# Optimization experiments

Hardware: AMD Instinct MI355X
Metric: run time of the kernel (lower is better)

Reference implementation:

```python
import jax, jax.numpy as jnp
import numpy as np

SCENE_BOUND = 1.5
INV_SCALE = 1.0 / (2.0 * np.sqrt(2.0))  # (1/sqrt(2))^3 per 3D haar synthesis step


def idwt3_haar(approx, details):
    """One level of 3D inverse Haar DWT.

    approx:  (C, D, D, D)   'aaa' subband
    details: (7, C, D, D, D) subbands in ptwt key order
             ('aad','ada','add','daa','dad','dda','ddd')
    returns: (C, 2D, 2D, 2D)
    """
    C, D = approx.shape[0], approx.shape[1]
    # Stack 8 subbands; key order is lexicographic in (a=0, d=1) per axis,
    # so reshape to a (2,2,2) subband grid indexed (b_depth, b_height, b_width).
    coeffs = jnp.concatenate([approx[None], details], axis=0).reshape(2, 2, 2, C, D, D, D)
    # Haar synthesis signs: approx contributes +1 to both output phases,
    # detail contributes +1 to even phase, -1 to odd phase.
    S = jnp.array([[1.0, 1.0], [1.0, -1.0]], dtype=approx.dtype)
    out = jnp.einsum('uvwcijk,up,vq,wr->cipjqkr', coeffs, S, S, S) * jnp.asarray(INV_SCALE, approx.dtype)
    return out.reshape(C, 2 * D, 2 * D, 2 * D)


def trilinear_query(vol, xyz, bound):
    """torch grid_sample(mode='bilinear', padding='zeros', align_corners=True).

    vol: (C, R, R, R) with dims (D, H, W); xyz: (N, 3) world coords,
    columns (x, y, z) index (W, H, D) respectively.
    returns: (N, C)
    """
    C, R = vol.shape[0], vol.shape[1]
    g = xyz / bound                                # normalized to [-1, 1]
    pix = (g + 1.0) * 0.5 * (R - 1)                # align_corners=True mapping
    i0 = jnp.floor(pix).astype(jnp.int32)
    frac = pix - i0.astype(vol.dtype)
    x0, y0, z0 = i0[:, 0], i0[:, 1], i0[:, 2]
    fx, fy, fz = frac[:, 0], frac[:, 1], frac[:, 2]

    def gather(ix, iy, iz):
        valid = ((ix >= 0) & (ix < R) & (iy >= 0) & (iy < R) & (iz >= 0) & (iz < R))
        v = vol[:, jnp.clip(iz, 0, R - 1), jnp.clip(iy, 0, R - 1), jnp.clip(ix, 0, R - 1)]  # (C, N)
        return v * valid.astype(vol.dtype)

    out = jnp.zeros((C, xyz.shape[0]), dtype=vol.dtype)
    for dz in (0, 1):
        wz = fz if dz else 1.0 - fz
        for dy in (0, 1):
            wy = fy if dy else 1.0 - fy
            for dx in (0, 1):
                wx = fx if dx else 1.0 - fx
                out = out + gather(x0 + dx, y0 + dy, z0 + dz) * (wx * wy * wz)
    return out.T  # (N, C)


def setup_inputs() -> dict:
    key = jax.random.key(0)
    k0, k1, k2, k3, k4 = jax.random.split(key, 5)
    C = 28
    approx = jax.random.normal(k0, (C, 16, 16, 16), dtype=jnp.float32) * 0.01
    details_0 = jax.random.normal(k1, (7, C, 16, 16, 16), dtype=jnp.float32) * 0.001
    details_1 = jax.random.normal(k2, (7, C, 32, 32, 32), dtype=jnp.float32) * 0.001
    details_2 = jax.random.normal(k3, (7, C, 64, 64, 64), dtype=jnp.float32) * 0.001
    xyz = (jax.random.uniform(k4, (1_000_000, 3), dtype=jnp.float32) * 2.0 - 1.0) * SCENE_BOUND
    return {"approx": approx, "details_0": details_0, "details_1": details_1,
            "details_2": details_2, "xyz": xyz}


def reference(approx, details_0, details_1, details_2, xyz):
    # reconstruct(max_level=None): incremental multi-level IDWT synthesis
    vol = approx
    for d in (details_0, details_1, details_2):
        vol = idwt3_haar(vol, d)          # (C, 32^3) -> (C, 64^3) -> (C, 128^3)
    # query(): trilinear interpolation at world-space points
    return trilinear_query(vol, xyz, SCENE_BOUND)  # (N, C)
```

## Files before the change

kernel.cpp:

```cpp
#include <hip/hip_runtime.h>
#include <hip/hip_fp16.h>

#define INVS 0.35355339059327373f
#define CCH 28
#define QRS 127

__device__ __forceinline__ void haar8(const float c[8], float o[8]) {
    float t00p = c[0] + c[1], t00m = c[0] - c[1];
    float t01p = c[2] + c[3], t01m = c[2] - c[3];
    float t10p = c[4] + c[5], t10m = c[4] - c[5];
    float t11p = c[6] + c[7], t11m = c[6] - c[7];
    float u00p = t00p + t01p, u00m = t00m + t01m;
    float u01p = t00p - t01p, u01m = t00m - t01m;
    float u10p = t10p + t11p, u10m = t10m + t11m;
    float u11p = t10p - t11p, u11m = t10m - t11m;
    o[0] = (u00p + u10p) * INVS;  o[1] = (u00m + u10m) * INVS;
    o[2] = (u01p + u11p) * INVS;  o[3] = (u01m + u11m) * INVS;
    o[4] = (u00p - u10p) * INVS;  o[5] = (u00m - u10m) * INVS;
    o[6] = (u01p - u11p) * INVS;  o[7] = (u01m - u11m) * INVS;
}

__device__ __forceinline__ float3 pixcoord(float x, float y, float z) {
    const float R1 = 63.5f, IB = 1.0f / 1.5f;
    float3 p;
    p.x = __fmul_rn(__fadd_rn(__fmul_rn(x, IB), 1.0f), R1);
    p.y = __fmul_rn(__fadd_rn(__fmul_rn(y, IB), 1.0f), R1);
    p.z = __fmul_rn(__fadd_rn(__fmul_rn(z, IB), 1.0f), R1);
    return p;
}
__device__ __forceinline__ int cell_of(float3 p) {
    int cx = min(max((int)floorf(p.x), 0), 127) >> 3;
    int cy = min(max((int)floorf(p.y), 0), 127) >> 3;
    int cz = min(max((int)floorf(p.z), 0), 127) >> 2;
    return (cz * 16 + cy) * 16 + cx;
}

template <int LOGD, typename TA>
__global__ void idwt_cf_h(const TA* __restrict__ approx,
                          const float* __restrict__ details,
                          __half* __restrict__ out) {
    constexpr int D  = 1 << LOGD;
    constexpr int D3 = D * D * D;
    int t  = blockIdx.x * blockDim.x + threadIdx.x;
    int xc = t & (D - 1);
    int yc = (t >> LOGD) & (D - 1);
    int zc = (t >> (2 * LOGD)) & (D - 1);
    int c  = t >> (3 * LOGD);
    if (c >= CCH) return;
    int base = c * D3 + ((zc * D + yc) * D + xc);
    float cf[8];
    cf[0] = (float)approx[base];
#pragma unroll
    for (int j = 0; j < 7; ++j) cf[j + 1] = details[j * (CCH * D3) + base];
    float o[8];
    haar8(cf, o);
    constexpr int D2 = 2 * D;
    __half2* outv = (__half2*)out;
    int ob = (((c * D2 + 2 * zc) * D2 + 2 * yc) * D + xc);
    __half2 h01, h23, h45, h67;
    h01.x = __float2half(o[0]); h01.y = __float2half(o[1]);
    h23.x = __float2half(o[2]); h23.y = __float2half(o[3]);
    h45.x = __float2half(o[4]); h45.y = __float2half(o[5]);
    h67.x = __float2half(o[6]); h67.y = __float2half(o[7]);
    outv[ob]              = h01;
    outv[ob + D]          = h23;
    outv[ob + D2 * D]     = h45;
    outv[ob + D2 * D + D] = h67;
}

__global__ void __launch_bounds__(256) idwt_last(const __half* __restrict__ vol1,
                                                 const float* __restrict__ details,
                                                 __half* __restrict__ out) {
    constexpr int D3 = 64 * 64 * 64;
    __shared__ unsigned short lds[4 * CCH * 130];
    int zc = blockIdx.x >> 6, yc = blockIdx.x & 63;
    int rowc = (zc * 64 + yc) * 64;
#pragma unroll 1
    for (int it = 0; it < 7; ++it) {
        int item = it * 256 + threadIdx.x;
        int c = item >> 6, xc = item & 63;
        int base = c * D3 + rowc + xc;
        float cf[8];
        cf[0] = (float)vol1[base];
#pragma unroll
        for (int j = 0; j < 7; ++j) cf[j + 1] = details[j * (CCH * D3) + base];
        float o[8];
        haar8(cf, o);
#pragma unroll
        for (int k = 0; k < 8; ++k) {
            int p2q = k >> 1, r = k & 1;
            lds[(p2q * CCH + c) * 130 + 2 * xc + r] = __half_as_ushort(__float2half(o[k]));
        }
    }
    __syncthreads();
#pragma unroll 1
    for (int it = 0; it < 7; ++it) {
        int t2 = it * 256 + threadIdx.x;
        int plane = t2 / 448;
        int rem = t2 - plane * 448;
        int p = plane >> 1, q = plane & 1;
        unsigned int h[8];
#pragma unroll
        for (int j = 0; j < 8; ++j) {
            int f = rem * 8 + j;
            int vox = f / 28;
            int ch = f - 28 * vox;
            h[j] = lds[(plane * CCH + ch) * 130 + vox];
        }
        uint4 r4;
        r4.x = h[0] | (h[1] << 16);
        r4.y = h[2] | (h[3] << 16);
        r4.z = h[4] | (h[5] << 16);
        r4.w = h[6] | (h[7] << 16);
        long orow = ((long)(2 * zc + p) * 128 + (2 * yc + q)) * (128 * CCH);
        ((uint4*)(out + orow))[rem] = r4;
    }
}

__global__ void hist_k(const float* __restrict__ xyz, int* __restrict__ hist, int N) {
    int i = blockIdx.x * 256 + threadIdx.x;
    if (i >= N) return;
    float3 p = pixcoord(xyz[3 * i], xyz[3 * i + 1], xyz[3 * i + 2]);
    atomicAdd(&hist[cell_of(p)], 1);
}

__global__ void __launch_bounds__(256) scan_k(const int* __restrict__ hist,
                                              int* __restrict__ off,
                                              int* __restrict__ cursor) {
    __shared__ int part[256];
    int t = threadIdx.x;
    int loc[32], s = 0;
#pragma unroll
    for (int i = 0; i < 32; ++i) { loc[i] = s; s += hist[t * 32 + i]; }
    part[t] = s;
    __syncthreads();
    for (int d = 1; d < 256; d <<= 1) {
        int v = (t >= d) ? part[t - d] : 0;
        __syncthreads();
        part[t] += v;
        __syncthreads();
    }
    int excl = part[t] - s;
#pragma unroll
    for (int i = 0; i < 32; ++i) {
        int o = excl + loc[i];
        off[t * 32 + i] = o;
        cursor[t * 32 + i] = o;
    }
    if (t == 255) off[8192] = part[255];
}

__global__ void scatter_k(const float* __restrict__ xyz, int* __restrict__ cursor,
                          float4* __restrict__ recs, int N) {
    int i = blockIdx.x * 256 + threadIdx.x;
    if (i >= N) return;
    float3 p = pixcoord(xyz[3 * i], xyz[3 * i + 1], xyz[3 * i + 2]);
    int cell = cell_of(p);
    int pos = atomicAdd(&cursor[cell], 1);
    recs[pos] = make_float4(__int_as_float(i), p.x, p.y, p.z);
}

__global__ void __launch_bounds__(256, 7) query_cell(const float4* __restrict__ recs,
                                                     const int* __restrict__ off,
                                                     const __half* __restrict__ vol,
                                                     float* __restrict__ out) {
    __shared__ unsigned int lds[45 * QRS];
    int cell = blockIdx.x;
    int cx = cell & 15, cy = (cell >> 4) & 15, cz = cell >> 8;
    const unsigned int* vd = (const unsigned int*)vol;
    const long VOLDW = 128L * 128 * 128 * 14;
    for (int e = threadIdx.x; e < 45 * 63; e += 256) {
        int row = e / 63;
        int k2  = e - row * 63;
        int lz = row / 9, ly = row - 9 * lz;
        int gz = min(4 * cz + lz, 127), gy = min(8 * cy + ly, 127);
        long g = ((long)(gz * 128 + gy) * 128 + 8 * cx) * 14 + 2 * k2;
        g = min(g, VOLDW - 2);
        uint2 v = *(const uint2*)(vd + g);
        lds[row * QRS + 2 * k2]     = v.x;
        lds[row * QRS + 2 * k2 + 1] = v.y;
    }
    __syncthreads();
    int i1 = off[cell + 1];
    for (int i = off[cell] + (int)threadIdx.x; i < i1; i += 256) {
        float4 r = recs[i];
        int q = __float_as_int(r.x);
        float px = r.y, py = r.z, pz = r.w;
        float flx = floorf(px), fly = floorf(py), flz = floorf(pz);
        int ix0 = (int)flx, iy0 = (int)fly, iz0 = (int)flz;
        float fx = px - flx, fy = py - fly, fz = pz - flz;
        float acc[CCH];
#pragma unroll
        for (int k = 0; k < CCH; ++k) acc[k] = 0.0f;
#pragma unroll
        for (int dz = 0; dz < 2; ++dz) {
            int iz = iz0 + dz;
            bool vz = (iz >= 0) & (iz < 128);
            float wz = dz ? fz : 1.0f - fz;
            int lzc = min(max(iz, 0), 127) - 4 * cz;
#pragma unroll
            for (int dy = 0; dy < 2; ++dy) {
                int iy = iy0 + dy;
                bool vy = (iy >= 0) & (iy < 128);
                float wy = dy ? fy : 1.0f - fy;
                int lyc = min(max(iy, 0), 127) - 8 * cy;
#pragma unroll
                for (int dx = 0; dx < 2; ++dx) {
                    int ix = ix0 + dx;
                    bool vx = (ix >= 0) & (ix < 128);
                    float wx = dx ? fx : 1.0f - fx;
                    int lxc = min(max(ix, 0), 127) - 8 * cx;
                    float w = (vx & vy & vz) ? (wx * wy * wz) : 0.0f;
                    const unsigned int* pr = &lds[(lzc * 9 + lyc) * QRS + 14 * lxc];
#pragma unroll
                    for (int j = 0; j < 7; ++j) {
                        unsigned int u0 = pr[2 * j], u1 = pr[2 * j + 1];
                        float2 f0 = __half22float2(*(__half2*)&u0);
                        float2 f1 = __half22float2(*(__half2*)&u1);
                        acc[4 * j + 0] += w * f0.x;
                        acc[4 * j + 1] += w * f0.y;
                        acc[4 * j + 2] += w * f1.x;
                        acc[4 * j + 3] += w * f1.y;
                    }
                }
            }
        }
        float4* o4 = (float4*)(out + (long)q * CCH);
#pragma unroll
        for (int j = 0; j < 7; ++j)
            o4[j] = make_float4(acc[4 * j], acc[4 * j + 1], acc[4 * j + 2], acc[4 * j + 3]);
    }
}

extern "C" void kernel_launch(void* const* d_in, const int* in_sizes, int n_in,
                              void* d_out, int out_size, void* d_ws, size_t ws_size,
                              hipStream_t stream) {
    const float* approx = (const float*)d_in[0];
    const float* det0   = (const float*)d_in[1];
    const float* det1   = (const float*)d_in[2];
    const float* det2   = (const float*)d_in[3];
    const float* xyz    = (const float*)d_in[4];
    int N = in_sizes[4] / 3;

    char* ws = (char*)d_ws;
    __half* vol0 = (__half*)ws;
    __half* vol1 = (__half*)(ws + 1835008);
    __half* vol2 = (__half*)(ws + 16515072);
    int*    hist = (int*)(ws + 133955584);
    int*    off  = (int*)(ws + 133988352);
    int*    curs = (int*)(ws + 134021136);
    float4* recs = (float4*)(ws + 134053904);

    hipMemsetAsync(hist, 0, 8192 * sizeof(int), stream);
    idwt_cf_h<4, float><<<448, 256, 0, stream>>>(approx, det0, vol0);
    idwt_cf_h<5, __half><<<3584, 256, 0, stream>>>(vol0, det1, vol1);
    idwt_last<<<4096, 256, 0, stream>>>(vol1, det2, vol2);
    int nb = (N + 255) / 256;
    hist_k<<<nb, 256, 0, stream>>>(xyz, hist, N);
    scan_k<<<1, 256, 0, stream>>>(hist, off, curs);
    scatter_k<<<nb, 256, 0, stream>>>(xyz, curs, recs, N);
    query_cell<<<8192, 256, 0, stream>>>(recs, off, vol2, (float*)d_out);
}
```

Measured before the change: 605.0 us.

## Vectorize mid-level IDWT, pack LDS half2 writes, and use nontemporal output stores

Replaces the second IDWT level with a kernel in which each thread handles two adjacent x voxels, using half2 and float2 loads and uint2 stores. In the last IDWT level, each thread now keeps a fixed x and loops over channel groups, and it writes packed half2 words to a 65-word-padded LDS array so scattered 16-bit stores become fewer 32-bit stores. The query kernel writes its output with nontemporal vector stores to avoid polluting the cache. Together these cut memory and LDS instruction counts, at the cost of more registers from the fully unrolled loops.

```diff
diff --git a/kernel.cpp b/kernel.cpp
--- a/kernel.cpp
+++ b/kernel.cpp
@@ -4,6 +4,8 @@
 #define INVS 0.35355339059327373f
 #define CCH 28
 #define QRS 127
+
+typedef float f32x4 __attribute__((ext_vector_type(4)));
 
 __device__ __forceinline__ void haar8(const float c[8], float o[8]) {
     float t00p = c[0] + c[1], t00m = c[0] - c[1];
@@ -68,17 +70,59 @@
     outv[ob + D2 * D + D] = h67;
 }
 
+__global__ void idwt_cf2(const __half* __restrict__ approx,
+                         const float* __restrict__ details,
+                         __half* __restrict__ out) {
+    constexpr int D = 32, D3 = D * D * D;
+    int t  = blockIdx.x * 256 + threadIdx.x;
+    int xp = t & 15;
+    int yc = (t >> 4) & 31;
+    int zc = (t >> 9) & 31;
+    int c  = t >> 14;
+    if (c >= CCH) return;
+    int base = c * D3 + ((zc * D + yc) * D + 2 * xp);
+    __half2 a2 = *(const __half2*)(approx + base);
+    float cfA[8], cfB[8];
+    cfA[0] = __half2float(a2.x);
+    cfB[0] = __half2float(a2.y);
+#pragma unroll
+    for (int j = 0; j < 7; ++j) {
+        float2 d2 = *(const float2*)(details + j * (CCH * D3) + base);
+        cfA[j + 1] = d2.x;
+        cfB[j + 1] = d2.y;
+    }
+    float oA[8], oB[8];
+    haar8(cfA, oA);
+    haar8(cfB, oB);
+    uint2* outv = (uint2*)out;
+#pragma unroll
+    for (int p = 0; p < 2; ++p)
+#pragma unroll
+        for (int q = 0; q < 2; ++q) {
+            int k0 = p * 4 + q * 2;
+            __half2 lo, hi;
+            lo.x = __float2half(oA[k0]);     lo.y = __float2half(oA[k0 + 1]);
+            hi.x = __float2half(oB[k0]);     hi.y = __float2half(oB[k0 + 1]);
+            uint2 v;
+            v.x = *(unsigned int*)&lo;
+            v.y = *(unsigned int*)&hi;
+            long oi = (((long)(c * 64 + 2 * zc + p) * 64 + 2 * yc + q) * 64 + 4 * xp) >> 2;
+            outv[oi] = v;
+        }
+}
+
 __global__ void __launch_bounds__(256) idwt_last(const __half* __restrict__ vol1,
                                                  const float* __restrict__ details,
                                                  __half* __restrict__ out) {
     constexpr int D3 = 64 * 64 * 64;
-    __shared__ unsigned short lds[4 * CCH * 130];
+    __shared__ unsigned int lds4[4 * CCH * 65];
+    unsigned short* lds = (unsigned short*)lds4;
     int zc = blockIdx.x >> 6, yc = blockIdx.x & 63;
     int rowc = (zc * 64 + yc) * 64;
-#pragma unroll 1
-    for (int it = 0; it < 7; ++it) {
-        int item = it * 256 + threadIdx.x;
-        int c = item >> 6, xc = item & 63;
+    int xc = threadIdx.x & 63, cg = threadIdx.x >> 6;
+#pragma unroll
+    for (int k = 0; k < 7; ++k) {
+        int c = cg + 4 * k;
         int base = c * D3 + rowc + xc;
         float cf[8];
         cf[0] = (float)vol1[base];
@@ -87,13 +131,15 @@
         float o[8];
         haar8(cf, o);
 #pragma unroll
-        for (int k = 0; k < 8; ++k) {
-            int p2q = k >> 1, r = k & 1;
-            lds[(p2q * CCH + c) * 130 + 2 * xc + r] = __half_as_ushort(__float2half(o[k]));
+        for (int m = 0; m < 4; ++m) {
+            __half2 h;
+            h.x = __float2half(o[2 * m]);
+            h.y = __float2half(o[2 * m + 1]);
+            lds4[(m * CCH + c) * 65 + xc] = *(unsigned int*)&h;
         }
     }
     __syncthreads();
-#pragma unroll 1
+#pragma unroll
     for (int it = 0; it < 7; ++it) {
         int t2 = it * 256 + threadIdx.x;
         int plane = t2 / 448;
@@ -225,10 +271,12 @@
                 }
             }
         }
-        float4* o4 = (float4*)(out + (long)q * CCH);
-#pragma unroll
-        for (int j = 0; j < 7; ++j)
-            o4[j] = make_float4(acc[4 * j], acc[4 * j + 1], acc[4 * j + 2], acc[4 * j + 3]);
+        f32x4* o4 = (f32x4*)(out + (long)q * CCH);
+#pragma unroll
+        for (int j = 0; j < 7; ++j) {
+            f32x4 v = {acc[4 * j], acc[4 * j + 1], acc[4 * j + 2], acc[4 * j + 3]};
+            __builtin_nontemporal_store(v, o4 + j);
+        }
     }
 }
 
@@ -253,7 +301,7 @@
 
     hipMemsetAsync(hist, 0, 8192 * sizeof(int), stream);
     idwt_cf_h<4, float><<<448, 256, 0, stream>>>(approx, det0, vol0);
-    idwt_cf_h<5, __half><<<3584, 256, 0, stream>>>(vol0, det1, vol1);
+    idwt_cf2<<<1792, 256, 0, stream>>>(vol0, det1, vol1);
     idwt_last<<<4096, 256, 0, stream>>>(vol1, det2, vol2);
     int nb = (N + 255) / 256;
     hist_k<<<nb, 256, 0, stream>>>(xyz, hist, N);
```

After: 750.4 us. +24.0%, slower.
